# Performance work log

Measured on AMD Instinct MI355X. Metric: run time of the kernel, lower is better.

## Reference

```python
import jax, jax.numpy as jnp
import numpy as np

HILBERT_BITS = 8
NDIM = 3


def hilbert_distance(grid, bits=HILBERT_BITS):
    """Vectorized Skilling transform: grid [..., 3] int32 in [0, 2**bits-1] -> Hilbert index [...] int32.
    Exact port of hilbertcurve.HilbertCurve.distance_from_point (n=3, p=bits)."""
    x = [grid[..., i] for i in range(NDIM)]
    m = 1 << (bits - 1)
    # Inverse undo excess work
    q = m
    while q > 1:
        pm = q - 1
        for i in range(NDIM):
            cond = (x[i] & q) != 0
            if i == 0:
                x[0] = jnp.where(cond, x[0] ^ pm, x[0])
            else:
                t = (x[0] ^ x[i]) & pm
                x0n = jnp.where(cond, x[0] ^ pm, x[0] ^ t)
                xin = jnp.where(cond, x[i], x[i] ^ t)
                x[0], x[i] = x0n, xin
        q >>= 1
    # Gray encode
    x[1] = x[1] ^ x[0]
    x[2] = x[2] ^ x[1]
    t = jnp.zeros_like(x[2])
    q = m
    while q > 1:
        t = jnp.where((x[2] & q) != 0, t ^ (q - 1), t)
        q >>= 1
    x = [xi ^ t for xi in x]
    # Interleave bits, MSB first, dim order 0,1,2 -> h has bits*3 bits (24 fits int32)
    h = jnp.zeros_like(x[0])
    for bpos in range(bits - 1, -1, -1):
        for i in range(NDIM):
            h = (h << 1) | ((x[i] >> bpos) & 1)
    return h


def hilbert_orders(x, bits=HILBERT_BITS):
    # x: [B, N, 3] float. Per-batch min/max normalization, then quantize to grid.
    mins = x.min(axis=1, keepdims=True)
    maxs = x.max(axis=1, keepdims=True)
    span = jnp.maximum(maxs - mins, 1e-6)
    norm = (x - mins) / span
    mx = (1 << bits) - 1
    grid_h = jnp.clip(norm * mx, 0, mx).astype(jnp.int32)
    grid_t = jnp.clip(norm[..., ::-1] * mx, 0, mx).astype(jnp.int32)  # [z,y,x] variant
    order_h = jnp.argsort(hilbert_distance(grid_h, bits), axis=-1)
    order_t = jnp.argsort(hilbert_distance(grid_t, bits), axis=-1)
    return order_h, order_t


def setup_inputs() -> dict:
    key = jax.random.key(0)
    k1, k2, k3 = jax.random.split(key, 3)
    B, N, D = 16, 4096, 384
    x = jax.random.normal(k1, (B, N, 3), dtype=jnp.float32)
    W = jax.random.normal(k2, (D, 3), dtype=jnp.float32) * 0.5
    b = jax.random.normal(k3, (D,), dtype=jnp.float32) * 0.1
    gamma = jnp.ones((2, D), dtype=jnp.float32)
    beta = jnp.zeros((2, D), dtype=jnp.float32)
    return {"x": x, "W": W, "b": b, "gamma": gamma, "beta": beta}


def reference(x, W, b, gamma, beta):
    order_h, order_t = hilbert_orders(x)                     # [B, N] each
    pts_h = jnp.take_along_axis(x, order_h[..., None], axis=1)  # [B, N, 3]
    pts_t = jnp.take_along_axis(x, order_t[..., None], axis=1)
    base_h = jnp.einsum('bnc,dc->bnd', pts_h, W) + b         # Linear(3, D)
    base_t = jnp.einsum('bnc,dc->bnd', pts_t, W) + b
    tokens_h = base_h * gamma[0] + beta[0]
    tokens_t = base_t * gamma[1] + beta[1]
    return jnp.concatenate([tokens_h, tokens_t], axis=1)     # [B, 2N, D]
```

## Files before the change

kernel.cpp:

```cpp
#include <hip/hip_runtime.h>
#include <stdint.h>

#define BATCH 16
#define NPTS 4096
#define DIM 384
#define NTOK (2*NPTS)
#define F4PT (DIM/4)

typedef unsigned long long u64;

__device__ __forceinline__ uint32_t spread3(uint32_t x) {
    x = (x | (x << 8)) & 0x00F00Fu;
    x = (x | (x << 4)) & 0x0C30C3u;
    x = (x | (x << 2)) & 0x249249u;
    return x;
}

__device__ __forceinline__ uint32_t hilbert3(uint32_t x0, uint32_t x1, uint32_t x2) {
    #pragma unroll
    for (uint32_t q = 128; q > 1; q >>= 1) {
        uint32_t pm = q - 1;
        if (x0 & q) x0 ^= pm;
        uint32_t t = (x0 ^ x1) & pm;
        if (x1 & q) { x0 ^= pm; } else { x0 ^= t; x1 ^= t; }
        t = (x0 ^ x2) & pm;
        if (x2 & q) { x0 ^= pm; } else { x0 ^= t; x2 ^= t; }
    }
    x1 ^= x0;
    x2 ^= x1;
    uint32_t t = 0;
    #pragma unroll
    for (uint32_t q = 128; q > 1; q >>= 1) { if (x2 & q) t ^= (q - 1); }
    x0 ^= t; x1 ^= t; x2 ^= t;
    return (spread3(x0) << 2) | (spread3(x1) << 1) | spread3(x2);
}

__global__ __launch_bounds__(512) void order_radix_o(const float* __restrict__ x,
                                                     u64* __restrict__ kws) {
    const int bi = blockIdx.x;
    const int b = bi >> 4;
    const int v = (bi >> 3) & 1;
    const int oct = bi & 7;
    const int t = threadIdx.x;
    const int lane = t & 63;
    const int w = t >> 6;

    __shared__ u64 skey[512];
    __shared__ uint32_t hist[3 * 2048];
    __shared__ uint32_t baseArr[256];
    __shared__ uint32_t waveTot[4];
    __shared__ float red[8 * 6];

    const float* xb = x + (size_t)b * NPTS * 3;
    const float4* xb4 = (const float4*)xb;

    float mnx = 1e30f, mny = 1e30f, mnz = 1e30f;
    float mxx = -1e30f, mxy = -1e30f, mxz = -1e30f;
    #pragma unroll
    for (int h = 0; h < 2; ++h) {
        float4 q0 = xb4[h * 1536 + 3 * t + 0];
        float4 q1 = xb4[h * 1536 + 3 * t + 1];
        float4 q2 = xb4[h * 1536 + 3 * t + 2];
        float px[4] = {q0.x, q0.w, q1.z, q2.y};
        float py[4] = {q0.y, q1.x, q1.w, q2.z};
        float pz[4] = {q0.z, q1.y, q2.x, q2.w};
        #pragma unroll
        for (int r = 0; r < 4; ++r) {
            mnx = fminf(mnx, px[r]); mxx = fmaxf(mxx, px[r]);
            mny = fminf(mny, py[r]); mxy = fmaxf(mxy, py[r]);
            mnz = fminf(mnz, pz[r]); mxz = fmaxf(mxz, pz[r]);
        }
    }
    #pragma unroll
    for (int off = 32; off > 0; off >>= 1) {
        mnx = fminf(mnx, __shfl_xor(mnx, off));
        mny = fminf(mny, __shfl_xor(mny, off));
        mnz = fminf(mnz, __shfl_xor(mnz, off));
        mxx = fmaxf(mxx, __shfl_xor(mxx, off));
        mxy = fmaxf(mxy, __shfl_xor(mxy, off));
        mxz = fmaxf(mxz, __shfl_xor(mxz, off));
    }
    if (lane == 0) {
        red[w*6+0] = mnx; red[w*6+1] = mny; red[w*6+2] = mnz;
        red[w*6+3] = mxx; red[w*6+4] = mxy; red[w*6+5] = mxz;
    }
    #pragma unroll
    for (int c = 0; c < 12; ++c) hist[t + c * 512] = 0u;
    __syncthreads();
    if (t == 0) {
        for (int ww = 1; ww < 8; ++ww) {
            mnx = fminf(mnx, red[ww*6+0]); mny = fminf(mny, red[ww*6+1]);
            mnz = fminf(mnz, red[ww*6+2]); mxx = fmaxf(mxx, red[ww*6+3]);
            mxy = fmaxf(mxy, red[ww*6+4]); mxz = fmaxf(mxz, red[ww*6+5]);
        }
        red[0] = mnx; red[1] = mny; red[2] = mnz;
        red[3] = fmaxf(mxx - mnx, 1e-6f);
        red[4] = fmaxf(mxy - mny, 1e-6f);
        red[5] = fmaxf(mxz - mnz, 1e-6f);
    }
    __syncthreads();
    mnx = red[0]; mny = red[1]; mnz = red[2];
    const float spx = red[3], spy = red[4], spz = red[5];

    u64 key;
    {
        const int n0 = (oct << 9) + t;
        float cx = xb[3*n0+0], cy = xb[3*n0+1], cz = xb[3*n0+2];
        float gx = fminf(fmaxf(((cx - mnx) / spx) * 255.0f, 0.0f), 255.0f);
        float gy = fminf(fmaxf(((cy - mny) / spy) * 255.0f, 0.0f), 255.0f);
        float gz = fminf(fmaxf(((cz - mnz) / spz) * 255.0f, 0.0f), 255.0f);
        uint32_t ix = (uint32_t)(int)gx;
        uint32_t iy = (uint32_t)(int)gy;
        uint32_t iz = (uint32_t)(int)gz;
        uint32_t a0 = v ? iz : ix;
        uint32_t a2 = v ? ix : iz;
        uint32_t code = hilbert3(a0, iy, a2);
        key = ((u64)code << 12) | (u64)n0;
    }

    const u64 below_mask = (1ull << lane) - 1ull;
    u64* segk = kws + (((b << 1) | v) << 12);

    #pragma unroll
    for (int p = 0; p < 3; ++p) {
        const int sh = 12 + 8 * p;
        uint32_t* histp = hist + p * 2048;

        unsigned d = (unsigned)(key >> sh) & 255u;
        u64 m = ~0ull;
        #pragma unroll
        for (int bit = 0; bit < 8; ++bit) {
            u64 bal = __ballot((int)((d >> bit) & 1u));
            m &= ((d >> bit) & 1u) ? bal : ~bal;
        }
        unsigned rk = (unsigned)__popcll(m & below_mask);
        if (rk == 0u)
            histp[d * 8 + w] = (unsigned)__popcll(m);
        __syncthreads();

        unsigned exclw = 0;
        if (t < 256) {
            uint32_t* hb = histp + t * 8;
            unsigned running = 0;
            #pragma unroll
            for (int s = 0; s < 8; ++s) {
                unsigned hv = hb[s];
                hb[s] = running;
                running += hv;
            }
            unsigned incl = running;
            #pragma unroll
            for (int off = 1; off < 64; off <<= 1) {
                unsigned nv = __shfl_up(incl, off);
                if (lane >= off) incl += nv;
            }
            if (lane == 63) waveTot[w] = incl;
            exclw = incl - running;
        }
        __syncthreads();

        if (t < 256) {
            unsigned base = exclw;
            #pragma unroll
            for (int ww = 0; ww < 4; ++ww)
                if (ww < w) base += waveTot[ww];
            baseArr[t] = base;
        }
        __syncthreads();

        unsigned pos = baseArr[d] + histp[d * 8 + w] + rk;

        if (p < 2) {
            skey[pos] = key;
            __syncthreads();
            key = skey[t];
        } else {
            segk[(oct << 9) + pos] = key;
        }
    }
}

__global__ __launch_bounds__(512) void merge_emit_kernel(const float* __restrict__ x,
                                                         const float* __restrict__ W,
                                                         const float* __restrict__ bias,
                                                         const float* __restrict__ gamma,
                                                         const float* __restrict__ beta,
                                                         const u64* __restrict__ kws,
                                                         float4* __restrict__ out4) {
    const int bi = blockIdx.x;
    const int b = bi >> 4;
    const int v = (bi >> 3) & 1;
    const int oct = bi & 7;
    const int t = threadIdx.x;

    __shared__ u64 runs[8 * 512];
    __shared__ __align__(16) float sw0[DIM], sw1[DIM], sw2[DIM], sc[DIM];
    __shared__ float cxs[512], cys[512], czs[512];
    __shared__ int rnk[512];

    if (t < DIM) {
        float g = gamma[v * DIM + t];
        sw0[t] = g * W[t*3+0];
        sw1[t] = g * W[t*3+1];
        sw2[t] = g * W[t*3+2];
        sc[t]  = g * bias[t] + beta[v * DIM + t];
    }

    const u64* segk = kws + (((b << 1) | v) << 12);
    #pragma unroll
    for (int j = 0; j < 8; ++j)
        runs[(j << 9) + t] = segk[(j << 9) + t];
    __syncthreads();

    u64 k = runs[(oct << 9) + t];
    int base7[7], c[7];
    #pragma unroll
    for (int j = 0; j < 7; ++j) {
        base7[j] = (j + (j >= oct ? 1 : 0)) << 9;
        c[j] = 0;
    }
    #pragma unroll
    for (int step = 512; step >= 1; step >>= 1) {
        #pragma unroll
        for (int j = 0; j < 7; ++j) {
            if (c[j] + step <= 512 && runs[base7[j] + c[j] + step - 1] < k)
                c[j] += step;
        }
    }
    int rank = t;
    #pragma unroll
    for (int j = 0; j < 7; ++j) rank += c[j];

    {
        int idx = (int)(k & 0xFFFull);
        const float* p = x + (size_t)b * NPTS * 3 + idx * 3;
        cxs[t] = p[0]; cys[t] = p[1]; czs[t] = p[2];
        rnk[t] = rank;
    }
    __syncthreads();

    const int tokbase = (b << 13) + (v << 12);
    for (int i = t; i < 512 * F4PT; i += 512) {
        int r = i / F4PT;
        int g = i - r * F4PT;
        float pxr = cxs[r], pyr = cys[r], pzr = czs[r];
        int d0 = g << 2;
        float4 w0 = *(const float4*)&sw0[d0];
        float4 w1 = *(const float4*)&sw1[d0];
        float4 w2 = *(const float4*)&sw2[d0];
        float4 cc = *(const float4*)&sc[d0];
        float4 o;
        o.x = pxr*w0.x + pyr*w1.x + pzr*w2.x + cc.x;
        o.y = pxr*w0.y + pyr*w1.y + pzr*w2.y + cc.y;
        o.z = pxr*w0.z + pyr*w1.z + pzr*w2.z + cc.z;
        o.w = pxr*w0.w + pyr*w1.w + pzr*w2.w + cc.w;
        out4[(size_t)(tokbase + rnk[r]) * F4PT + g] = o;
    }
}

extern "C" void kernel_launch(void* const* d_in, const int* in_sizes, int n_in,
                              void* d_out, int out_size, void* d_ws, size_t ws_size,
                              hipStream_t stream) {
    const float* x     = (const float*)d_in[0];
    const float* W     = (const float*)d_in[1];
    const float* bias  = (const float*)d_in[2];
    const float* gamma = (const float*)d_in[3];
    const float* beta  = (const float*)d_in[4];

    u64* kws = (u64*)d_ws;

    hipLaunchKernelGGL(order_radix_o,     dim3(BATCH * 16), dim3(512), 0, stream, x, kws);
    hipLaunchKernelGGL(merge_emit_kernel, dim3(BATCH * 16), dim3(512), 0, stream,
                       x, W, bias, gamma, beta, kws, (float4*)d_out);
}
```

Measured before the change: 50.84 us.

## Fuse radix-sort and merge-emit kernels with per-segment spin barrier

```diff
diff --git a/kernel.cpp b/kernel.cpp
--- a/kernel.cpp
+++ b/kernel.cpp
@@ -35,8 +35,28 @@
     return (spread3(x0) << 2) | (spread3(x1) << 1) | spread3(x2);
 }
 
-__global__ __launch_bounds__(512) void order_radix_o(const float* __restrict__ x,
-                                                     u64* __restrict__ kws) {
+struct S1 {
+    u64 skey[512];
+    uint32_t hist[3 * 2048];
+    uint32_t baseArr[256];
+    uint32_t waveTot[4];
+    float red[8 * 6];
+};
+struct S2 {
+    u64 runs[8 * 512];
+    float cxs[512], cys[512], czs[512];
+    int rnk[512];
+};
+union ShU { S1 a; S2 b; };
+
+__global__ __launch_bounds__(512) void fused_kernel(const float* __restrict__ x,
+                                                    const float* __restrict__ W,
+                                                    const float* __restrict__ bias,
+                                                    const float* __restrict__ gamma,
+                                                    const float* __restrict__ beta,
+                                                    u64* __restrict__ kws,
+                                                    int* __restrict__ done,
+                                                    float4* __restrict__ out4) {
     const int bi = blockIdx.x;
     const int b = bi >> 4;
     const int v = (bi >> 3) & 1;
@@ -45,14 +65,19 @@
     const int lane = t & 63;
     const int w = t >> 6;
 
-    __shared__ u64 skey[512];
-    __shared__ uint32_t hist[3 * 2048];
-    __shared__ uint32_t baseArr[256];
-    __shared__ uint32_t waveTot[4];
-    __shared__ float red[8 * 6];
+    __shared__ ShU sh;
+    __shared__ __align__(16) float sw0[DIM], sw1[DIM], sw2[DIM], sc[DIM];
 
     const float* xb = x + (size_t)b * NPTS * 3;
     const float4* xb4 = (const float4*)xb;
+
+    if (t < DIM) {
+        float g = gamma[v * DIM + t];
+        sw0[t] = g * W[t*3+0];
+        sw1[t] = g * W[t*3+1];
+        sw2[t] = g * W[t*3+2];
+        sc[t]  = g * bias[t] + beta[v * DIM + t];
+    }
 
     float mnx = 1e30f, mny = 1e30f, mnz = 1e30f;
     float mxx = -1e30f, mxy = -1e30f, mxz = -1e30f;
@@ -81,26 +106,26 @@
         mxz = fmaxf(mxz, __shfl_xor(mxz, off));
     }
     if (lane == 0) {
-        red[w*6+0] = mnx; red[w*6+1] = mny; red[w*6+2] = mnz;
-        red[w*6+3] = mxx; red[w*6+4] = mxy; red[w*6+5] = mxz;
-    }
-    #pragma unroll
-    for (int c = 0; c < 12; ++c) hist[t + c * 512] = 0u;
+        sh.a.red[w*6+0] = mnx; sh.a.red[w*6+1] = mny; sh.a.red[w*6+2] = mnz;
+        sh.a.red[w*6+3] = mxx; sh.a.red[w*6+4] = mxy; sh.a.red[w*6+5] = mxz;
+    }
+    #pragma unroll
+    for (int c = 0; c < 12; ++c) sh.a.hist[t + c * 512] = 0u;
     __syncthreads();
     if (t == 0) {
         for (int ww = 1; ww < 8; ++ww) {
-            mnx = fminf(mnx, red[ww*6+0]); mny = fminf(mny, red[ww*6+1]);
-            mnz = fminf(mnz, red[ww*6+2]); mxx = fmaxf(mxx, red[ww*6+3]);
-            mxy = fmaxf(mxy, red[ww*6+4]); mxz = fmaxf(mxz, red[ww*6+5]);
-        }
-        red[0] = mnx; red[1] = mny; red[2] = mnz;
-        red[3] = fmaxf(mxx - mnx, 1e-6f);
-        red[4] = fmaxf(mxy - mny, 1e-6f);
-        red[5] = fmaxf(mxz - mnz, 1e-6f);
-    }
-    __syncthreads();
-    mnx = red[0]; mny = red[1]; mnz = red[2];
-    const float spx = red[3], spy = red[4], spz = red[5];
+            mnx = fminf(mnx, sh.a.red[ww*6+0]); mny = fminf(mny, sh.a.red[ww*6+1]);
+            mnz = fminf(mnz, sh.a.red[ww*6+2]); mxx = fmaxf(mxx, sh.a.red[ww*6+3]);
+            mxy = fmaxf(mxy, sh.a.red[ww*6+4]); mxz = fmaxf(mxz, sh.a.red[ww*6+5]);
+        }
+        sh.a.red[0] = mnx; sh.a.red[1] = mny; sh.a.red[2] = mnz;
+        sh.a.red[3] = fmaxf(mxx - mnx, 1e-6f);
+        sh.a.red[4] = fmaxf(mxy - mny, 1e-6f);
+        sh.a.red[5] = fmaxf(mxz - mnz, 1e-6f);
+    }
+    __syncthreads();
+    mnx = sh.a.red[0]; mny = sh.a.red[1]; mnz = sh.a.red[2];
+    const float spx = sh.a.red[3], spy = sh.a.red[4], spz = sh.a.red[5];
 
     u64 key;
     {
@@ -120,13 +145,14 @@
 
     const u64 below_mask = (1ull << lane) - 1ull;
     u64* segk = kws + (((b << 1) | v) << 12);
+    const int g = (b << 1) | v;
 
     #pragma unroll
     for (int p = 0; p < 3; ++p) {
-        const int sh = 12 + 8 * p;
-        uint32_t* histp = hist + p * 2048;
-
-        unsigned d = (unsigned)(key >> sh) & 255u;
+        const int sh4 = 12 + 8 * p;
+        uint32_t* histp = sh.a.hist + p * 2048;
+
+        unsigned d = (unsigned)(key >> sh4) & 255u;
         u64 m = ~0ull;
         #pragma unroll
         for (int bit = 0; bit < 8; ++bit) {
@@ -154,7 +180,7 @@
                 unsigned nv = __shfl_up(incl, off);
                 if (lane >= off) incl += nv;
             }
-            if (lane == 63) waveTot[w] = incl;
+            if (lane == 63) sh.a.waveTot[w] = incl;
             exclw = incl - running;
         }
         __syncthreads();
@@ -163,56 +189,38 @@
             unsigned base = exclw;
             #pragma unroll
             for (int ww = 0; ww < 4; ++ww)
-                if (ww < w) base += waveTot[ww];
-            baseArr[t] = base;
+                if (ww < w) base += sh.a.waveTot[ww];
+            sh.a.baseArr[t] = base;
         }
         __syncthreads();
 
-        unsigned pos = baseArr[d] + histp[d * 8 + w] + rk;
+        unsigned pos = sh.a.baseArr[d] + histp[d * 8 + w] + rk;
 
         if (p < 2) {
-            skey[pos] = key;
+            sh.a.skey[pos] = key;
             __syncthreads();
-            key = skey[t];
+            key = sh.a.skey[t];
         } else {
             segk[(oct << 9) + pos] = key;
         }
     }
-}
-
-__global__ __launch_bounds__(512) void merge_emit_kernel(const float* __restrict__ x,
-                                                         const float* __restrict__ W,
-                                                         const float* __restrict__ bias,
-                                                         const float* __restrict__ gamma,
-                                                         const float* __restrict__ beta,
-                                                         const u64* __restrict__ kws,
-                                                         float4* __restrict__ out4) {
-    const int bi = blockIdx.x;
-    const int b = bi >> 4;
-    const int v = (bi >> 3) & 1;
-    const int oct = bi & 7;
-    const int t = threadIdx.x;
-
-    __shared__ u64 runs[8 * 512];
-    __shared__ __align__(16) float sw0[DIM], sw1[DIM], sw2[DIM], sc[DIM];
-    __shared__ float cxs[512], cys[512], czs[512];
-    __shared__ int rnk[512];
-
-    if (t < DIM) {
-        float g = gamma[v * DIM + t];
-        sw0[t] = g * W[t*3+0];
-        sw1[t] = g * W[t*3+1];
-        sw2[t] = g * W[t*3+2];
-        sc[t]  = g * bias[t] + beta[v * DIM + t];
-    }
-
-    const u64* segk = kws + (((b << 1) | v) << 12);
+
+    __threadfence();
+    __syncthreads();
+    if (t == 0) {
+        atomicAdd(&done[g], 1);
+        while (atomicAdd(&done[g], 0) < 8)
+            __builtin_amdgcn_s_sleep(8);
+    }
+    __syncthreads();
+    __threadfence();
+
     #pragma unroll
     for (int j = 0; j < 8; ++j)
-        runs[(j << 9) + t] = segk[(j << 9) + t];
-    __syncthreads();
-
-    u64 k = runs[(oct << 9) + t];
+        sh.b.runs[(j << 9) + t] = segk[(j << 9) + t];
+    __syncthreads();
+
+    u64 k = sh.b.runs[(oct << 9) + t];
     int base7[7], c[7];
     #pragma unroll
     for (int j = 0; j < 7; ++j) {
@@ -223,7 +231,7 @@
     for (int step = 512; step >= 1; step >>= 1) {
         #pragma unroll
         for (int j = 0; j < 7; ++j) {
-            if (c[j] + step <= 512 && runs[base7[j] + c[j] + step - 1] < k)
+            if (c[j] + step <= 512 && sh.b.runs[base7[j] + c[j] + step - 1] < k)
                 c[j] += step;
         }
     }
@@ -233,18 +241,18 @@
 
     {
         int idx = (int)(k & 0xFFFull);
-        const float* p = x + (size_t)b * NPTS * 3 + idx * 3;
-        cxs[t] = p[0]; cys[t] = p[1]; czs[t] = p[2];
-        rnk[t] = rank;
+        const float* p = xb + idx * 3;
+        sh.b.cxs[t] = p[0]; sh.b.cys[t] = p[1]; sh.b.czs[t] = p[2];
+        sh.b.rnk[t] = rank;
     }
     __syncthreads();
 
     const int tokbase = (b << 13) + (v << 12);
     for (int i = t; i < 512 * F4PT; i += 512) {
         int r = i / F4PT;
-        int g = i - r * F4PT;
-        float pxr = cxs[r], pyr = cys[r], pzr = czs[r];
-        int d0 = g << 2;
+        int gg = i - r * F4PT;
+        float pxr = sh.b.cxs[r], pyr = sh.b.cys[r], pzr = sh.b.czs[r];
+        int d0 = gg << 2;
         float4 w0 = *(const float4*)&sw0[d0];
         float4 w1 = *(const float4*)&sw1[d0];
         float4 w2 = *(const float4*)&sw2[d0];
@@ -254,7 +262,7 @@
         o.y = pxr*w0.y + pyr*w1.y + pzr*w2.y + cc.y;
         o.z = pxr*w0.z + pyr*w1.z + pzr*w2.z + cc.z;
         o.w = pxr*w0.w + pyr*w1.w + pzr*w2.w + cc.w;
-        out4[(size_t)(tokbase + rnk[r]) * F4PT + g] = o;
+        out4[(size_t)(tokbase + sh.b.rnk[r]) * F4PT + gg] = o;
     }
 }
 
@@ -267,9 +275,10 @@
     const float* gamma = (const float*)d_in[3];
     const float* beta  = (const float*)d_in[4];
 
-    u64* kws = (u64*)d_ws;
-
-    hipLaunchKernelGGL(order_radix_o,     dim3(BATCH * 16), dim3(512), 0, stream, x, kws);
-    hipLaunchKernelGGL(merge_emit_kernel, dim3(BATCH * 16), dim3(512), 0, stream,
-                       x, W, bias, gamma, beta, kws, (float4*)d_out);
-}
+    u64* kws  = (u64*)d_ws;
+    int* done = (int*)(kws + 32 * 4096);
+
+    hipMemsetAsync(done, 0, 32 * sizeof(int), stream);
+    hipLaunchKernelGGL(fused_kernel, dim3(BATCH * 16), dim3(512), 0, stream,
+                       x, W, bias, gamma, beta, kws, done, (float4*)d_out);
+}
```

Result: slower. 158.7 us (+212.2%).

## Split sort into 16 runs of 256 per batch-variant with 512 smaller blocks

Applied to the files above, without the earlier changes.

```diff
diff --git a/kernel.cpp b/kernel.cpp
--- a/kernel.cpp
+++ b/kernel.cpp
@@ -6,6 +6,8 @@
 #define DIM 384
 #define NTOK (2*NPTS)
 #define F4PT (DIM/4)
+#define NRUN 16
+#define RUN 256
 
 typedef unsigned long long u64;
 
@@ -35,21 +37,21 @@
     return (spread3(x0) << 2) | (spread3(x1) << 1) | spread3(x2);
 }
 
-__global__ __launch_bounds__(512) void order_radix_o(const float* __restrict__ x,
+__global__ __launch_bounds__(256) void order_radix_s(const float* __restrict__ x,
                                                      u64* __restrict__ kws) {
     const int bi = blockIdx.x;
-    const int b = bi >> 4;
-    const int v = (bi >> 3) & 1;
-    const int oct = bi & 7;
+    const int b = bi >> 5;
+    const int v = (bi >> 4) & 1;
+    const int sed = bi & 15;
     const int t = threadIdx.x;
     const int lane = t & 63;
     const int w = t >> 6;
 
-    __shared__ u64 skey[512];
-    __shared__ uint32_t hist[3 * 2048];
+    __shared__ u64 skey[RUN];
+    __shared__ uint32_t hist[3 * 1024];
     __shared__ uint32_t baseArr[256];
     __shared__ uint32_t waveTot[4];
-    __shared__ float red[8 * 6];
+    __shared__ float red[4 * 6];
 
     const float* xb = x + (size_t)b * NPTS * 3;
     const float4* xb4 = (const float4*)xb;
@@ -57,10 +59,10 @@
     float mnx = 1e30f, mny = 1e30f, mnz = 1e30f;
     float mxx = -1e30f, mxy = -1e30f, mxz = -1e30f;
     #pragma unroll
-    for (int h = 0; h < 2; ++h) {
-        float4 q0 = xb4[h * 1536 + 3 * t + 0];
-        float4 q1 = xb4[h * 1536 + 3 * t + 1];
-        float4 q2 = xb4[h * 1536 + 3 * t + 2];
+    for (int g = 0; g < 4; ++g) {
+        float4 q0 = xb4[12*t + 3*g + 0];
+        float4 q1 = xb4[12*t + 3*g + 1];
+        float4 q2 = xb4[12*t + 3*g + 2];
         float px[4] = {q0.x, q0.w, q1.z, q2.y};
         float py[4] = {q0.y, q1.x, q1.w, q2.z};
         float pz[4] = {q0.z, q1.y, q2.x, q2.w};
@@ -85,10 +87,10 @@
         red[w*6+3] = mxx; red[w*6+4] = mxy; red[w*6+5] = mxz;
     }
     #pragma unroll
-    for (int c = 0; c < 12; ++c) hist[t + c * 512] = 0u;
+    for (int c = 0; c < 12; ++c) hist[t + c * 256] = 0u;
     __syncthreads();
     if (t == 0) {
-        for (int ww = 1; ww < 8; ++ww) {
+        for (int ww = 1; ww < 4; ++ww) {
             mnx = fminf(mnx, red[ww*6+0]); mny = fminf(mny, red[ww*6+1]);
             mnz = fminf(mnz, red[ww*6+2]); mxx = fmaxf(mxx, red[ww*6+3]);
             mxy = fmaxf(mxy, red[ww*6+4]); mxz = fmaxf(mxz, red[ww*6+5]);
@@ -104,7 +106,7 @@
 
     u64 key;
     {
-        const int n0 = (oct << 9) + t;
+        const int n0 = (sed << 8) + t;
         float cx = xb[3*n0+0], cy = xb[3*n0+1], cz = xb[3*n0+2];
         float gx = fminf(fmaxf(((cx - mnx) / spx) * 255.0f, 0.0f), 255.0f);
         float gy = fminf(fmaxf(((cy - mny) / spy) * 255.0f, 0.0f), 255.0f);
@@ -124,7 +126,7 @@
     #pragma unroll
     for (int p = 0; p < 3; ++p) {
         const int sh = 12 + 8 * p;
-        uint32_t* histp = hist + p * 2048;
+        uint32_t* histp = hist + p * 1024;
 
         unsigned d = (unsigned)(key >> sh) & 255u;
         u64 m = ~0ull;
@@ -135,15 +137,15 @@
         }
         unsigned rk = (unsigned)__popcll(m & below_mask);
         if (rk == 0u)
-            histp[d * 8 + w] = (unsigned)__popcll(m);
+            histp[d * 4 + w] = (unsigned)__popcll(m);
         __syncthreads();
 
-        unsigned exclw = 0;
-        if (t < 256) {
-            uint32_t* hb = histp + t * 8;
+        unsigned exclw;
+        {
+            uint32_t* hb = histp + t * 4;
             unsigned running = 0;
             #pragma unroll
-            for (int s = 0; s < 8; ++s) {
+            for (int s = 0; s < 4; ++s) {
                 unsigned hv = hb[s];
                 hb[s] = running;
                 running += hv;
@@ -159,7 +161,7 @@
         }
         __syncthreads();
 
-        if (t < 256) {
+        {
             unsigned base = exclw;
             #pragma unroll
             for (int ww = 0; ww < 4; ++ww)
@@ -168,19 +170,19 @@
         }
         __syncthreads();
 
-        unsigned pos = baseArr[d] + histp[d * 8 + w] + rk;
+        unsigned pos = baseArr[d] + histp[d * 4 + w] + rk;
 
         if (p < 2) {
             skey[pos] = key;
             __syncthreads();
             key = skey[t];
         } else {
-            segk[(oct << 9) + pos] = key;
-        }
-    }
-}
-
-__global__ __launch_bounds__(512) void merge_emit_kernel(const float* __restrict__ x,
+            segk[(sed << 8) + pos] = key;
+        }
+    }
+}
+
+__global__ __launch_bounds__(256) void merge_emit_kernel(const float* __restrict__ x,
                                                          const float* __restrict__ W,
                                                          const float* __restrict__ bias,
                                                          const float* __restrict__ gamma,
@@ -188,15 +190,15 @@
                                                          const u64* __restrict__ kws,
                                                          float4* __restrict__ out4) {
     const int bi = blockIdx.x;
-    const int b = bi >> 4;
-    const int v = (bi >> 3) & 1;
-    const int oct = bi & 7;
+    const int b = bi >> 5;
+    const int v = (bi >> 4) & 1;
+    const int sed = bi & 15;
     const int t = threadIdx.x;
 
-    __shared__ u64 runs[8 * 512];
+    __shared__ u64 runs[NRUN * RUN];
     __shared__ __align__(16) float sw0[DIM], sw1[DIM], sw2[DIM], sc[DIM];
-    __shared__ float cxs[512], cys[512], czs[512];
-    __shared__ int rnk[512];
+    __shared__ float cxs[RUN], cys[RUN], czs[RUN];
+    __shared__ int rnk[RUN];
 
     if (t < DIM) {
         float g = gamma[v * DIM + t];
@@ -205,31 +207,39 @@
         sw2[t] = g * W[t*3+2];
         sc[t]  = g * bias[t] + beta[v * DIM + t];
     }
+    if (t + 256 < DIM) {
+        int i = t + 256;
+        float g = gamma[v * DIM + i];
+        sw0[i] = g * W[i*3+0];
+        sw1[i] = g * W[i*3+1];
+        sw2[i] = g * W[i*3+2];
+        sc[i]  = g * bias[i] + beta[v * DIM + i];
+    }
 
     const u64* segk = kws + (((b << 1) | v) << 12);
     #pragma unroll
-    for (int j = 0; j < 8; ++j)
-        runs[(j << 9) + t] = segk[(j << 9) + t];
-    __syncthreads();
-
-    u64 k = runs[(oct << 9) + t];
-    int base7[7], c[7];
-    #pragma unroll
-    for (int j = 0; j < 7; ++j) {
-        base7[j] = (j + (j >= oct ? 1 : 0)) << 9;
+    for (int j = 0; j < NRUN; ++j)
+        runs[(j << 8) + t] = segk[(j << 8) + t];
+    __syncthreads();
+
+    u64 k = runs[(sed << 8) + t];
+    int base15[15], c[15];
+    #pragma unroll
+    for (int j = 0; j < 15; ++j) {
+        base15[j] = (j + (j >= sed ? 1 : 0)) << 8;
         c[j] = 0;
     }
     #pragma unroll
-    for (int step = 512; step >= 1; step >>= 1) {
+    for (int step = RUN; step >= 1; step >>= 1) {
         #pragma unroll
-        for (int j = 0; j < 7; ++j) {
-            if (c[j] + step <= 512 && runs[base7[j] + c[j] + step - 1] < k)
+        for (int j = 0; j < 15; ++j) {
+            if (c[j] + step <= RUN && runs[base15[j] + c[j] + step - 1] < k)
                 c[j] += step;
         }
     }
     int rank = t;
     #pragma unroll
-    for (int j = 0; j < 7; ++j) rank += c[j];
+    for (int j = 0; j < 15; ++j) rank += c[j];
 
     {
         int idx = (int)(k & 0xFFFull);
@@ -240,7 +250,7 @@
     __syncthreads();
 
     const int tokbase = (b << 13) + (v << 12);
-    for (int i = t; i < 512 * F4PT; i += 512) {
+    for (int i = t; i < RUN * F4PT; i += 256) {
         int r = i / F4PT;
         int g = i - r * F4PT;
         float pxr = cxs[r], pyr = cys[r], pzr = czs[r];
@@ -269,7 +279,7 @@
 
     u64* kws = (u64*)d_ws;
 
-    hipLaunchKernelGGL(order_radix_o,     dim3(BATCH * 16), dim3(512), 0, stream, x, kws);
-    hipLaunchKernelGGL(merge_emit_kernel, dim3(BATCH * 16), dim3(512), 0, stream,
+    hipLaunchKernelGGL(order_radix_s,     dim3(BATCH * 32), dim3(256), 0, stream, x, kws);
+    hipLaunchKernelGGL(merge_emit_kernel, dim3(BATCH * 32), dim3(256), 0, stream,
                        x, W, bias, gamma, beta, kws, (float4*)d_out);
 }
```

After: 54.36 us. 1.07x slower.
